# Performance work log

Hardware: AMD Instinct MI355X
Metric: run time of the kernel (lower is better)

Reference implementation:

```python
import jax, jax.numpy as jnp
import numpy as np

B, L, E, H = 2, 2048, 1024, 16
D = E // H  # 64


def setup_inputs() -> dict:
    key = jax.random.key(0)
    ks = jax.random.split(key, 9)
    return {
        "query": jax.random.normal(ks[0], (B, L, E), dtype=jnp.float32),
        "value": jax.random.normal(ks[1], (B, L, E), dtype=jnp.float32),
        "key": jax.random.normal(ks[2], (B, L, E), dtype=jnp.float32),
        "mask": jax.random.randint(ks[3], (B, 1, L, L), 0, 2, dtype=jnp.int32),
        "Wq": jax.random.normal(ks[4], (D, D), dtype=jnp.float32) * 0.05,
        "Wk": jax.random.normal(ks[5], (D, D), dtype=jnp.float32) * 0.05,
        "Wv": jax.random.normal(ks[6], (D, D), dtype=jnp.float32) * 0.05,
        "Wfc": jax.random.normal(ks[7], (E, E), dtype=jnp.float32) * 0.02,
        "bfc": jax.random.normal(ks[8], (E,), dtype=jnp.float32) * 0.02,
    }


def reference(query, value, key, mask, Wq, Wk, Wv, Wfc, bfc):
    b, q_len, _ = query.shape
    k_len = key.shape[1]
    v_len = value.shape[1]
    # split heads: [b, l, H, D]
    q = query.reshape(b, q_len, H, D)
    k = key.reshape(b, k_len, H, D)
    v = value.reshape(b, v_len, H, D)
    # per-head linear projections (shared weights across heads, no bias)
    q = jnp.einsum('bqhd,ed->bqhe', q, Wq)
    k = jnp.einsum('bkhd,ed->bkhe', k, Wk)
    v = jnp.einsum('bvhd,ed->bvhe', v, Wv)
    # attention scores [b, H, q, k]
    attn = jnp.einsum('bqhd,bkhd->bhqk', q, k)
    # NOTE: original masks BEFORE scaling, and scales by sqrt(embedding_size)
    attn = jnp.where(mask == 0, jnp.float32(-1e20), attn)
    attn = attn / jnp.float32(E ** 0.5)
    attn = jax.nn.softmax(attn, axis=3)
    out = jnp.einsum('bhqk,bkhd->bqhd', attn, v).reshape(b, q_len, E)
    out = out @ Wfc.T + bfc
    return out
```

## Files before the change

### kernel.cpp

```cpp
#include <hip/hip_runtime.h>
#include <hip/hip_bf16.h>


#define B_ 2
#define L_ 2048
#define E_ 1024
#define H_ 16
#define D_ 64

typedef __attribute__((ext_vector_type(8))) short s8v;
typedef __attribute__((ext_vector_type(4))) float f4v;
typedef __attribute__((ext_vector_type(2))) float f2v;

__device__ __forceinline__ f4v mfma16(s8v a, s8v b, f4v c) {
    return __builtin_amdgcn_mfma_f32_16x16x32_bf16(a, b, c, 0, 0, 0);
}

__device__ __forceinline__ float fast_exp2(float x) {
    return __builtin_amdgcn_exp2f(x);
}

__device__ __forceinline__ ushort bf16bits(float f) {
    __hip_bfloat16 h = __float2bfloat16(f);
    return *(ushort*)&h;
}

__device__ __forceinline__ void glds16(const __hip_bfloat16* g, ushort* l) {
    __builtin_amdgcn_global_load_lds(
        (const __attribute__((address_space(1))) void*)g,
        (__attribute__((address_space(3))) void*)l,
        16, 0, 0);
}

__device__ __forceinline__ s8v ld8_dual(const void* p, size_t idx, bool isf32) {
    if (isf32) {
        const float* pf = (const float*)p + idx;
        f4v f0 = *(const f4v*)pf;
        f4v f1 = *(const f4v*)(pf + 4);
        s8v r;
        r[0] = (short)bf16bits(f0[0]); r[1] = (short)bf16bits(f0[1]);
        r[2] = (short)bf16bits(f0[2]); r[3] = (short)bf16bits(f0[3]);
        r[4] = (short)bf16bits(f1[0]); r[5] = (short)bf16bits(f1[1]);
        r[6] = (short)bf16bits(f1[2]); r[7] = (short)bf16bits(f1[3]);
        return r;
    }
    return *(const s8v*)((const __hip_bfloat16*)p + idx);
}

__device__ __forceinline__ s8v ld8_ws(const __hip_bfloat16* p) {
    return *(const s8v*)p;
}

__device__ __forceinline__ s8v u4_to_s8(uint a, uint b, uint c, uint d) {
    union { uint u[4]; s8v v; } x;
    x.u[0] = a; x.u[1] = b; x.u[2] = c; x.u[3] = d;
    return x.v;
}

__device__ __forceinline__ bool block_detect_f32(const void* q_in, int* sflag) {
    if (threadIdx.x == 0) *sflag = 0;
    __syncthreads();
    const ushort* qq = (const ushort*)q_in + (threadIdx.x & 255) * 16;
    int bad = 0;
    #pragma unroll
    for (int i = 0; i < 16; ++i) bad += (((qq[i] >> 7) & 0xFF) >= 0x8E);
    bad += __shfl_xor(bad, 1);
    bad += __shfl_xor(bad, 2);
    bad += __shfl_xor(bad, 4);
    bad += __shfl_xor(bad, 8);
    bad += __shfl_xor(bad, 16);
    bad += __shfl_xor(bad, 32);
    if ((threadIdx.x & 63) == 0 && threadIdx.x < 256) atomicAdd(sflag, bad);
    __syncthreads();
    return *sflag > 100;
}

__device__ __forceinline__ void cvt_piece(
    size_t i4, const void* Wfc, const void* bfc,
    __hip_bfloat16* wfc_bf, __hip_bfloat16* bfc_bf, bool isf32)
{
    const size_t base = i4 * 4;
    const size_t n1 = (size_t)E_ * E_;
    if (base >= n1 + E_) return;
    const void* src = (base < n1) ? Wfc : bfc;
    const size_t off = (base < n1) ? base : base - n1;
    __hip_bfloat16* dst = (base < n1) ? (wfc_bf + off) : (bfc_bf + off);
    if (isf32) {
        f4v v = *(const f4v*)((const float*)src + off);
        #pragma unroll
        for (int j = 0; j < 4; ++j) dst[j] = __float2bfloat16(v[j]);
    } else {
        *(ushort4*)dst = *(const ushort4*)((const ushort*)src + off);
    }
}

__global__ __launch_bounds__(256) void proj_all_kernel(
    const void* __restrict__ q_in, const void* __restrict__ k_in,
    const void* __restrict__ v_in,
    const void* __restrict__ Wq, const void* __restrict__ Wk,
    const void* __restrict__ Wv,
    const void* __restrict__ Wfc, const void* __restrict__ bfc,
    const int* __restrict__ mask, unsigned long long* __restrict__ mbits,
    __hip_bfloat16* __restrict__ qp, __hip_bfloat16* __restrict__ kp,
    __hip_bfloat16* __restrict__ vpT,
    __hip_bfloat16* __restrict__ wfc_bf, __hip_bfloat16* __restrict__ bfc_bf)
{
    __shared__ __align__(16) ushort tile[64][72];
    __shared__ __align__(16) ushort wlds[64 * 72];
    __shared__ int sflag;
    const int wave = threadIdx.x >> 6;
    const int lane = threadIdx.x & 63;
    const int quad = lane >> 4;
    const int l16  = lane & 15;

    if (blockIdx.y == 3) {
        const int lane_ = threadIdx.x & 63;
        const size_t wbase = (size_t)blockIdx.x * 128 + wave * 32;
        #pragma unroll 4
        for (int i = 0; i < 32; ++i) {
            const size_t widx = wbase + i;
            const int v = mask[widx * 64 + lane_];
            const unsigned long long bal = __ballot(v != 0);
            if (lane_ == 0) mbits[widx] = bal;
        }
        return;
    }

    const bool isf32 = block_detect_f32(q_in, &sflag);

    if (blockIdx.y == 4) {
        cvt_piece((size_t)blockIdx.x * 256 + threadIdx.x, Wfc, bfc, wfc_bf, bfc_bf, isf32);
        if (blockIdx.x == 0)
            cvt_piece((size_t)(E_ * (size_t)E_ / 4) + threadIdx.x, Wfc, bfc, wfc_bf, bfc_bf, isf32);
        return;
    }

    {
        const void* W = blockIdx.y == 0 ? Wq : (blockIdx.y == 1 ? Wk : Wv);
        const int row = threadIdx.x >> 2;
        const int c0  = (threadIdx.x & 3) * 16;
        if (isf32) {
            const float* wsrc = (const float*)W + row * 64 + c0;
            #pragma unroll
            for (int j = 0; j < 16; ++j)
                wlds[row * 72 + c0 + j] = bf16bits(wsrc[j]);
        } else {
            const ushort* wsrc = (const ushort*)W + row * 64 + c0;
            *(s8v*)&wlds[row * 72 + c0]     = *(const s8v*)wsrc;
            *(s8v*)&wlds[row * 72 + c0 + 8] = *(const s8v*)(wsrc + 8);
        }
    }
    __syncthreads();

    if (blockIdx.y < 2) {
        const void* X = blockIdx.y == 0 ? q_in : k_in;
        __hip_bfloat16* dst = blockIdx.y == 0 ? qp : kp;
        const float oscale = (blockIdx.y == 0) ? 0.045084439755930314f : 1.0f;
        const int m0 = (blockIdx.x * 4 + wave) * 16;

        const size_t abase = (size_t)(m0 + l16) * D_;
        s8v a0 = ld8_dual(X, abase + quad * 8, isf32);
        s8v a1 = ld8_dual(X, abase + 32 + quad * 8, isf32);

        f4v acc[4];
        #pragma unroll
        for (int nt = 0; nt < 4; ++nt) {
            const ushort* wr = &wlds[(nt * 16 + l16) * 72];
            s8v b0 = *(const s8v*)(wr + quad * 8);
            s8v b1 = *(const s8v*)(wr + 32 + quad * 8);
            f4v c = {0.f, 0.f, 0.f, 0.f};
            c = mfma16(a0, b0, c);
            c = mfma16(a1, b1, c);
            acc[nt] = c;
        }
        #pragma unroll
        for (int r = 0; r < 4; ++r) {
            const int m = m0 + quad * 4 + r;
            const int h = m & 15;
            const int bl = m >> 4;
            const int b = bl >> 11;
            const int l = bl & (L_ - 1);
            #pragma unroll
            for (int nt = 0; nt < 4; ++nt) {
                const int e = nt * 16 + l16;
                dst[(((size_t)(b * H_ + h)) * L_ + l) * D_ + e] =
                    __float2bfloat16(acc[nt][r] * oscale);
            }
        }
    } else {
        const int l0 = (blockIdx.x & 31) * 64;
        const int bh = blockIdx.x >> 5;
        const int b = bh >> 4, h = bh & 15;
        const int lw = l0 + wave * 16;

        const size_t xbase = ((size_t)(b * L_ + lw + l16)) * E_ + h * D_;
        s8v a0 = ld8_dual(v_in, xbase + quad * 8, isf32);
        s8v a1 = ld8_dual(v_in, xbase + 32 + quad * 8, isf32);

        #pragma unroll
        for (int nt = 0; nt < 4; ++nt) {
            const int e = nt * 16 + l16;
            const ushort* wr = &wlds[e * 72];
            s8v b0 = *(const s8v*)(wr + quad * 8);
            s8v b1 = *(const s8v*)(wr + 32 + quad * 8);
            f4v c = {0.f, 0.f, 0.f, 0.f};
            c = mfma16(a0, b0, c);
            c = mfma16(a1, b1, c);
            #pragma unroll
            for (int r = 0; r < 4; ++r)
                tile[wave * 16 + quad * 4 + r][e] = bf16bits(c[r]);
        }
        __syncthreads();
        const int e  = threadIdx.x >> 2;
        const int lc = (threadIdx.x & 3) * 16;
        s8v s0, s1;
        #pragma unroll
        for (int i = 0; i < 8; ++i) {
            s0[i] = (short)tile[lc + i][e];
            s1[i] = (short)tile[lc + 8 + i][e];
        }
        __hip_bfloat16* drow = vpT + ((size_t)bh * D_ + e) * L_ + l0 + lc;
        *(s8v*)drow = s0;
        *(s8v*)(drow + 8) = s1;
    }
}

__global__ __launch_bounds__(256) void cvt_wfc_kernel(
    const void* __restrict__ Wfc, const void* __restrict__ bfc,
    __hip_bfloat16* __restrict__ wfc_bf, __hip_bfloat16* __restrict__ bfc_bf,
    const void* __restrict__ q_in)
{
    __shared__ int sflag;
    const bool isf32 = block_detect_f32(q_in, &sflag);
    cvt_piece((size_t)blockIdx.x * 256 + threadIdx.x, Wfc, bfc, wfc_bf, bfc_bf, isf32);
}

__global__ __launch_bounds__(512, 2) void attn_kernel(
    const __hip_bfloat16* __restrict__ qp,
    const __hip_bfloat16* __restrict__ kp,
    const __hip_bfloat16* __restrict__ vpT,
    const unsigned long long* __restrict__ mbits,
    __hip_bfloat16* __restrict__ attn_out)
{
    __shared__ __align__(16) ushort kv[2][2][64 * 64];

    const int wave = threadIdx.x >> 6;
    const int lane = threadIdx.x & 63;
    const int quad = lane >> 4;
    const int l16  = lane & 15;
    const int sw   = l16 & 7;
    const int bh = blockIdx.y;
    const int b = bh >> 4, h = bh & 15;
    const int q0 = blockIdx.x * 128 + wave * 16;

    const __hip_bfloat16* kbh = kp + (size_t)bh * L_ * D_;
    const __hip_bfloat16* vbh = vpT + (size_t)bh * D_ * L_;
    const unsigned long long* mrow = mbits + ((size_t)b * L_ + q0 + l16) * 32;

    const int lrow = lane >> 3;
    const int lchk = (lane & 7) ^ lrow;
    const int r0 = wave * 8;
    const __hip_bfloat16* kg = kbh + (size_t)(r0 + lrow) * D_ + lchk * 8;
    const __hip_bfloat16* vg = vbh + (size_t)(r0 + lrow) * L_ + lchk * 8;

    const __hip_bfloat16* qbase = qp + ((size_t)bh * L_ + q0) * D_;
    s8v qa0 = ld8_ws(qbase + (size_t)l16 * D_ + quad * 8);
    s8v qa1 = ld8_ws(qbase + (size_t)l16 * D_ + 32 + quad * 8);

    f2v rs2 = {0.f, 0.f};
    f4v o[4];
    #pragma unroll
    for (int nt = 0; nt < 4; ++nt) o[nt] = (f4v){0.f, 0.f, 0.f, 0.f};

    const int ro0 = l16 * 64 + ((quad ^ sw) << 3);
    const int ro1 = l16 * 64 + (((quad + 4) ^ sw) << 3);
    const int shq = quad * 4;

    glds16(kg, &kv[0][0][r0 * 64]);
    glds16(vg, &kv[0][1][r0 * 64]);
    kg += 64 * D_; vg += 64;
    __syncthreads();

#define ATTN_BODY(IT_, CUR_, PRE_)                                             \
    {                                                                          \
        const unsigned long long wq = mrow[(IT_)];                             \
        const uint wlo_sh = ((uint)wq) >> shq;                                 \
        const uint whi_sh = ((uint)(wq >> 32)) >> shq;                         \
        if (PRE_) {                                                            \
            glds16(kg, &kv[(CUR_) ^ 1][0][r0 * 64]);                           \
            glds16(vg, &kv[(CUR_) ^ 1][1][r0 * 64]);                           \
            kg += 64 * D_; vg += 64;                                           \
        }                                                                      \
        f4v s_[4];                                                             \
        __builtin_amdgcn_s_setprio(1);                                         \
        _Pragma("unroll")                                                      \
        for (int nt = 0; nt < 4; ++nt) {                                       \
            s8v kb0 = *(const s8v*)&kv[(CUR_)][0][nt * 1024 + ro0];            \
            s8v kb1 = *(const s8v*)&kv[(CUR_)][0][nt * 1024 + ro1];            \
            f4v c = {0.f, 0.f, 0.f, 0.f};                                      \
            c = mfma16(kb0, qa0, c);                                           \
            c = mfma16(kb1, qa1, c);                                           \
            s_[nt] = c;                                                        \
        }                                                                      \
        __builtin_amdgcn_s_setprio(0);                                         \
        uint dw[4][2];                                                         \
        _Pragma("unroll")                                                      \
        for (int nt = 0; nt < 4; ++nt) {                                       \
            const uint hs = (nt & 2) ? whi_sh : wlo_sh;                        \
            float pr[4];                                                       \
            _Pragma("unroll")                                                  \
            for (int r = 0; r < 4; ++r) {                                      \
                const float p = fast_exp2(s_[nt][r]);                          \
                const int m = __builtin_amdgcn_sbfe((int)hs,                   \
                                  ((nt & 1) << 4) + r, 1);                     \
                pr[r] = __uint_as_float(__float_as_uint(p) & (uint)m);         \
            }                                                                  \
            rs2 += (f2v){pr[0], pr[1]};                                        \
            rs2 += (f2v){pr[2], pr[3]};                                        \
            asm("v_cvt_pk_bf16_f32 %0, %1, %2"                                 \
                : "=v"(dw[nt][0]) : "v"(pr[0]), "v"(pr[1]));                   \
            asm("v_cvt_pk_bf16_f32 %0, %1, %2"                                 \
                : "=v"(dw[nt][1]) : "v"(pr[2]), "v"(pr[3]));                   \
        }                                                                      \
        uint w00 = dw[0][0], w10 = dw[1][0];                                   \
        uint w01 = dw[0][1], w11 = dw[1][1];                                   \
        uint w20 = dw[2][0], w30 = dw[3][0];                                   \
        uint w21 = dw[2][1], w31 = dw[3][1];                                   \
        asm("v_permlane32_swap_b32 %0, %1" : "+v"(w00), "+v"(w10));            \
        asm("v_permlane16_swap_b32 %0, %1" : "+v"(w00), "+v"(w10));            \
        asm("v_permlane32_swap_b32 %0, %1" : "+v"(w01), "+v"(w11));            \
        asm("v_permlane16_swap_b32 %0, %1" : "+v"(w01), "+v"(w11));            \
        asm("v_permlane32_swap_b32 %0, %1" : "+v"(w20), "+v"(w30));            \
        asm("v_permlane16_swap_b32 %0, %1" : "+v"(w20), "+v"(w30));            \
        asm("v_permlane32_swap_b32 %0, %1" : "+v"(w21), "+v"(w31));            \
        asm("v_permlane16_swap_b32 %0, %1" : "+v"(w21), "+v"(w31));            \
        s8v pa0 = u4_to_s8(w00, w01, w10, w11);                                \
        s8v pa1 = u4_to_s8(w20, w21, w30, w31);                                \
        __builtin_amdgcn_s_setprio(1);                                         \
        _Pragma("unroll")                                                      \
        for (int nt = 0; nt < 4; ++nt) {                                       \
            s8v vb0 = *(const s8v*)&kv[(CUR_)][1][nt * 1024 + ro0];            \
            s8v vb1 = *(const s8v*)&kv[(CUR_)][1][nt * 1024 + ro1];            \
            o[nt] = mfma16(pa0, vb0, o[nt]);                                   \
            o[nt] = mfma16(pa1, vb1, o[nt]);                                   \
        }                                                                      \
        __builtin_amdgcn_s_setprio(0);                                         \
        __syncthreads();                                                       \
    }

    for (int it2 = 0; it2 < 15; ++it2) {
        ATTN_BODY(2 * it2, 0, true)
        ATTN_BODY(2 * it2 + 1, 1, true)
    }
    ATTN_BODY(30, 0, true)
    ATTN_BODY(31, 1, false)
#undef ATTN_BODY

    float v = rs2[0] + rs2[1];
    v += __shfl_xor(v, 16, 64);
    v += __shfl_xor(v, 32, 64);
    #pragma unroll
    for (int r = 0; r < 4; ++r) {
        const int qrow = quad * 4 + r;
        const float li = __shfl(v, qrow, 64);
        const float inv = 1.0f / fmaxf(li, 1e-30f);
        const int row = q0 + qrow;
        #pragma unroll
        for (int nt = 0; nt < 4; ++nt) {
            const int d = nt * 16 + l16;
            attn_out[((size_t)(b * L_ + row)) * E_ + h * D_ + d] =
                __float2bfloat16(o[nt][r] * inv);
        }
    }
}

__global__ __launch_bounds__(256, 4) void fc_kernel(
    const __hip_bfloat16* __restrict__ x,
    const __hip_bfloat16* __restrict__ wfc_bf,
    const __hip_bfloat16* __restrict__ bfc_bf,
    void* __restrict__ out, const void* __restrict__ q_in)
{
    __shared__ __align__(16) ushort abuf[2][128 * 64];
    __shared__ __align__(16) ushort bbuf[2][64 * 64];
    __shared__ int sflag;
    const bool isf32 = block_detect_f32(q_in, &sflag);
    const int wave = threadIdx.x >> 6;
    const int lane = threadIdx.x & 63;
    const int quad = lane >> 4;
    const int l16  = lane & 15;
    const int sw   = l16 & 7;
    const int m0 = blockIdx.x * 128;
    const int n0 = blockIdx.y * 64;
    const int wr = wave >> 1;
    const int wc = wave & 1;

    const int lrow = lane >> 3;
    const int lchk = (lane & 7) ^ lrow;

    const __hip_bfloat16* ag[4];
    #pragma unroll
    for (int c = 0; c < 4; ++c)
        ag[c] = x + (size_t)(m0 + c * 32 + wave * 8 + lrow) * E_ + lchk * 8;
    const __hip_bfloat16* bg[2];
    #pragma unroll
    for (int c = 0; c < 2; ++c)
        bg[c] = wfc_bf + (size_t)(n0 + c * 32 + wave * 8 + lrow) * E_ + lchk * 8;

    f4v acc[4][2];
    #pragma unroll
    for (int fm = 0; fm < 4; ++fm)
        #pragma unroll
        for (int fn = 0; fn < 2; ++fn) acc[fm][fn] = (f4v){0.f, 0.f, 0.f, 0.f};

    #pragma unroll
    for (int c = 0; c < 4; ++c) glds16(ag[c], &abuf[0][(c * 32 + wave * 8) * 64]);
    #pragma unroll
    for (int c = 0; c < 2; ++c) glds16(bg[c], &bbuf[0][(c * 32 + wave * 8) * 64]);
    __syncthreads();

    int cur = 0;
    for (int it = 0; it < 16; ++it) {
        if (it < 15) {
            #pragma unroll
            for (int c = 0; c < 4; ++c)
                glds16(ag[c] + (it + 1) * 64, &abuf[cur ^ 1][(c * 32 + wave * 8) * 64]);
            #pragma unroll
            for (int c = 0; c < 2; ++c)
                glds16(bg[c] + (it + 1) * 64, &bbuf[cur ^ 1][(c * 32 + wave * 8) * 64]);
        }
        s8v a0[4], a1[4];
        #pragma unroll
        for (int fm = 0; fm < 4; ++fm) {
            const ushort* ar = &abuf[cur][(wr * 64 + fm * 16 + l16) * 64];
            a0[fm] = *(const s8v*)(ar + ((quad ^ sw) << 3));
            a1[fm] = *(const s8v*)(ar + (((quad + 4) ^ sw) << 3));
        }
        #pragma unroll
        for (int fn = 0; fn < 2; ++fn) {
            const ushort* br = &bbuf[cur][(wc * 32 + fn * 16 + l16) * 64];
            s8v b0 = *(const s8v*)(br + ((quad ^ sw) << 3));
            s8v b1 = *(const s8v*)(br + (((quad + 4) ^ sw) << 3));
            #pragma unroll
            for (int fm = 0; fm < 4; ++fm) {
                acc[fm][fn] = mfma16(a0[fm], b0, acc[fm][fn]);
                acc[fm][fn] = mfma16(a1[fm], b1, acc[fm][fn]);
            }
        }
        __syncthreads();
        cur ^= 1;
    }
    #pragma unroll
    for (int fm = 0; fm < 4; ++fm) {
        #pragma unroll
        for (int r = 0; r < 4; ++r) {
            const int m = m0 + wr * 64 + fm * 16 + quad * 4 + r;
            #pragma unroll
            for (int fn = 0; fn < 2; ++fn) {
                const int n = n0 + wc * 32 + fn * 16 + l16;
                const float val = acc[fm][fn][r] + __bfloat162float(bfc_bf[n]);
                if (isf32) ((float*)out)[(size_t)m * E_ + n] = val;
                else       ((__hip_bfloat16*)out)[(size_t)m * E_ + n] = __float2bfloat16(val);
            }
        }
    }
}

extern "C" void kernel_launch(void* const* d_in, const int* in_sizes, int n_in,
                              void* d_out, int out_size, void* d_ws, size_t ws_size,
                              hipStream_t stream) {
    const void* query = d_in[0];
    const void* value = d_in[1];
    const void* key   = d_in[2];
    const int*  mask  = (const int*)d_in[3];
    const void* Wq  = d_in[4];
    const void* Wk  = d_in[5];
    const void* Wv  = d_in[6];
    const void* Wfc = d_in[7];
    const void* bfc = d_in[8];

    char* ws = (char*)d_ws;
    unsigned long long* mbits     = (unsigned long long*)(ws + (64u << 10));
    __hip_bfloat16* qp            = (__hip_bfloat16*)(ws + (2u  << 20));
    __hip_bfloat16* kp            = (__hip_bfloat16*)(ws + (10u << 20));
    __hip_bfloat16* vpT           = (__hip_bfloat16*)(ws + (18u << 20));
    __hip_bfloat16* attn_out      = (__hip_bfloat16*)(ws + (26u << 20));

    const bool big_ws = ws_size >= (37ull << 20);
    __hip_bfloat16* wfc_bf = big_ws ? (__hip_bfloat16*)(ws + (34ull << 20)) : qp;
    __hip_bfloat16* bfc_bf = wfc_bf + (size_t)E_ * E_;

    proj_all_kernel<<<dim3(1024, big_ws ? 5 : 4), 256, 0, stream>>>(
        query, key, value, Wq, Wk, Wv, Wfc, bfc, mask, mbits,
        qp, kp, vpT, wfc_bf, bfc_bf);
    attn_kernel<<<dim3(16, 32), 512, 0, stream>>>(qp, kp, vpT, mbits, attn_out);
    if (!big_ws)
        cvt_wfc_kernel<<<1025, 256, 0, stream>>>(Wfc, bfc, wfc_bf, bfc_bf, query);
    fc_kernel<<<dim3(32, 16), 256, 0, stream>>>(attn_out, wfc_bf, bfc_bf, d_out, query);
}
```

Baseline: 218.2 us.

## Deepen K/V LDS pipeline to four stages with explicit vmcnt waits

Grows the shared K/V ring from two buffers to four, keeping two tiles of prefetch in flight, and prefetches the mask words two iterations ahead into registers. It replaces the end-of-iteration __syncthreads with a manual s_waitcnt vmcnt plus s_barrier at the start of each iteration, aiming to hide global-to-LDS latency better. LDS per block doubles to 64KB, which may limit occupancy at two blocks per CU. The hand-counted vmcnt values rely on the exact number of outstanding loads, which makes the change fragile.

```diff
diff --git a/kernel.cpp b/kernel.cpp
--- a/kernel.cpp
+++ b/kernel.cpp
@@ -242,7 +242,7 @@
     const unsigned long long* __restrict__ mbits,
     __hip_bfloat16* __restrict__ attn_out)
 {
-    __shared__ __align__(16) ushort kv[2][2][64 * 64];
+    __shared__ __align__(16) ushort kv[4][2][64 * 64];
 
     const int wave = threadIdx.x >> 6;
     const int lane = threadIdx.x & 63;
@@ -276,27 +276,36 @@
     const int ro1 = l16 * 64 + (((quad + 4) ^ sw) << 3);
     const int shq = quad * 4;
 
+    unsigned long long wq0 = 0, wq1 = 0, wq2 = 0, wq3 = 0;
+
     glds16(kg, &kv[0][0][r0 * 64]);
     glds16(vg, &kv[0][1][r0 * 64]);
+    wq0 = mrow[0];
     kg += 64 * D_; vg += 64;
-    __syncthreads();
-
-#define ATTN_BODY(IT_, CUR_, PRE_)                                             \
+    glds16(kg, &kv[1][0][r0 * 64]);
+    glds16(vg, &kv[1][1][r0 * 64]);
+    wq1 = mrow[1];
+    kg += 64 * D_; vg += 64;
+
+#define ATTN_BODY(IT_, CUR_, DST_, PRE_, VMASM_)                               \
     {                                                                          \
-        const unsigned long long wq = mrow[(IT_)];                             \
-        const uint wlo_sh = ((uint)wq) >> shq;                                 \
-        const uint whi_sh = ((uint)(wq >> 32)) >> shq;                         \
         if (PRE_) {                                                            \
-            glds16(kg, &kv[(CUR_) ^ 1][0][r0 * 64]);                           \
-            glds16(vg, &kv[(CUR_) ^ 1][1][r0 * 64]);                           \
+            glds16(kg, &kv[DST_][0][r0 * 64]);                                 \
+            glds16(vg, &kv[DST_][1][r0 * 64]);                                 \
+            wq##DST_ = mrow[(IT_) + 2];                                        \
             kg += 64 * D_; vg += 64;                                           \
         }                                                                      \
+        asm volatile(VMASM_ ::: "memory");                                     \
+        __builtin_amdgcn_s_barrier();                                          \
+        __builtin_amdgcn_sched_barrier(0);                                     \
+        const uint wlo_sh = ((uint)wq##CUR_) >> shq;                           \
+        const uint whi_sh = ((uint)(wq##CUR_ >> 32)) >> shq;                   \
         f4v s_[4];                                                             \
         __builtin_amdgcn_s_setprio(1);                                         \
         _Pragma("unroll")                                                      \
         for (int nt = 0; nt < 4; ++nt) {                                       \
-            s8v kb0 = *(const s8v*)&kv[(CUR_)][0][nt * 1024 + ro0];            \
-            s8v kb1 = *(const s8v*)&kv[(CUR_)][0][nt * 1024 + ro1];            \
+            s8v kb0 = *(const s8v*)&kv[CUR_][0][nt * 1024 + ro0];              \
+            s8v kb1 = *(const s8v*)&kv[CUR_][0][nt * 1024 + ro1];              \
             f4v c = {0.f, 0.f, 0.f, 0.f};                                      \
             c = mfma16(kb0, qa0, c);                                           \
             c = mfma16(kb1, qa1, c);                                           \
@@ -339,21 +348,25 @@
         __builtin_amdgcn_s_setprio(1);                                         \
         _Pragma("unroll")                                                      \
         for (int nt = 0; nt < 4; ++nt) {                                       \
-            s8v vb0 = *(const s8v*)&kv[(CUR_)][1][nt * 1024 + ro0];            \
-            s8v vb1 = *(const s8v*)&kv[(CUR_)][1][nt * 1024 + ro1];            \
+            s8v vb0 = *(const s8v*)&kv[CUR_][1][nt * 1024 + ro0];              \
+            s8v vb1 = *(const s8v*)&kv[CUR_][1][nt * 1024 + ro1];              \
             o[nt] = mfma16(pa0, vb0, o[nt]);                                   \
             o[nt] = mfma16(pa1, vb1, o[nt]);                                   \
         }                                                                      \
         __builtin_amdgcn_s_setprio(0);                                         \
-        __syncthreads();                                                       \
-    }
-
-    for (int it2 = 0; it2 < 15; ++it2) {
-        ATTN_BODY(2 * it2, 0, true)
-        ATTN_BODY(2 * it2 + 1, 1, true)
-    }
-    ATTN_BODY(30, 0, true)
-    ATTN_BODY(31, 1, false)
+    }
+
+    for (int it4 = 0; it4 < 7; ++it4) {
+        const int t = it4 * 4;
+        ATTN_BODY(t,     0, 2, true, "s_waitcnt vmcnt(6)")
+        ATTN_BODY(t + 1, 1, 3, true, "s_waitcnt vmcnt(6)")
+        ATTN_BODY(t + 2, 2, 0, true, "s_waitcnt vmcnt(6)")
+        ATTN_BODY(t + 3, 3, 1, true, "s_waitcnt vmcnt(6)")
+    }
+    ATTN_BODY(28, 0, 2, true,  "s_waitcnt vmcnt(6)")
+    ATTN_BODY(29, 1, 3, true,  "s_waitcnt vmcnt(6)")
+    ATTN_BODY(30, 2, 0, false, "s_waitcnt vmcnt(3)")
+    ATTN_BODY(31, 3, 1, false, "s_waitcnt vmcnt(0)")
 #undef ATTN_BODY
 
     float v = rs2[0] + rs2[1];
```

Result: no change. 214.2 us (median of 3 runs) (-1.8%).
